# Performance work log

Hardware: AMD Instinct MI355X
Metric: run time of the kernel (lower is better)

The kernel has to match this reference:

```python
import jax, jax.numpy as jnp
import numpy as np

OUT, L, LPS, K = 256, 24, 6, 3          # classes, layers, layers_per_stack, kernel
RC, GC, SC, FC = 64, 128, 64, 80        # residual, gate, skip, feature channels
SCALES = (4, 4, 4, 4)                   # upsample scales, prod = 256 (hop size)
AUX = 2                                 # aux_context_window
B, T = 2, 16384
TF = T // int(np.prod(SCALES)) + 2 * AUX  # 68 mel frames fed in


def _conv1d(x, w, b=None, dilation=1, pad=(0, 0)):
    # x: (B,C,T), w: (O,C,K)
    y = jax.lax.conv_general_dilated(x, w, (1,), [pad], rhs_dilation=(dilation,),
                                     dimension_numbers=('NCH', 'OIH', 'NCH'))
    return y if b is None else y + b[None, :, None]


def _smooth(x, k):
    # depthwise-in-time smoothing: Conv2d(1,1,(1,Kk)) applied to (B,1,C,T)
    Bb, C, Tt = x.shape
    Kk = k.shape[0]
    y = jax.lax.conv_general_dilated(x.reshape(Bb * C, 1, Tt), k.reshape(1, 1, Kk),
                                     (1,), [(Kk // 2, Kk // 2)],
                                     dimension_numbers=('NCH', 'OIH', 'NCH'))
    return y.reshape(Bb, C, Tt)


def _wavenet(x, feature, first_W, first_b, conv_W, conv_b, cond_W,
             skip_W, skip_b, res_W, res_b, last1_W, last1_b, last2_W, last2_b,
             convin_W, up_K):
    # shift right by one (teacher forcing) then one-hot -> (B, OUT, T)
    xs = jnp.pad(x, ((0, 0), (1, 0)))[:, :-1]
    xoh = jax.nn.one_hot(xs, OUT, dtype=jnp.float32).transpose(0, 2, 1)

    # ConvInUpsampleNetwork: valid conv over aux context, then nearest-up + smooth
    f = _conv1d(feature, convin_W)  # (B, FC, TF - 2*AUX)
    for i, s in enumerate(SCALES):
        f = jnp.repeat(f, s, axis=-1)
        f = _smooth(f, up_K[i])
    # f: (B, FC, T)

    out = jnp.einsum('oc,bct->bot', first_W, xoh) + first_b[None, :, None]
    skips = jnp.zeros((x.shape[0], SC, x.shape[1]), jnp.float32)
    for l in range(L):
        d = 2 ** (l % LPS)
        pad = (K - 1) * d  # causal: left-pad only (== torch pad both + trim right)
        h = _conv1d(out, conv_W[l], conv_b[l], dilation=d, pad=(pad, 0))
        h = h + jnp.einsum('oc,bct->bot', cond_W[l], f)
        a, g = jnp.split(h, 2, axis=1)
        z = jnp.tanh(a) * jax.nn.sigmoid(g)  # (B, GC//2, T)
        skips = skips + jnp.einsum('oc,bct->bot', skip_W[l], z) + skip_b[l][None, :, None]
        out = jnp.einsum('oc,bct->bot', res_W[l], z) + res_b[l][None, :, None] + out
    h = jax.nn.relu(skips)
    h = jax.nn.relu(jnp.einsum('oc,bct->bot', last1_W, h) + last1_b[None, :, None])
    h = jnp.einsum('oc,bct->bot', last2_W, h) + last2_b[None, :, None]
    return h  # (B, OUT, T)


def setup_inputs() -> dict:
    key = jax.random.key(0)
    ks = jax.random.split(key, 12)
    s = 0.05
    return {
        'x': jax.random.randint(ks[0], (B, T), 0, OUT),
        'feature': jax.random.normal(ks[1], (B, FC, TF), jnp.float32),
        'first_W': jax.random.normal(ks[2], (RC, OUT), jnp.float32) * s,
        'first_b': jnp.zeros((RC,), jnp.float32),
        'conv_W': jax.random.normal(ks[3], (L, GC, RC, K), jnp.float32) * s,
        'conv_b': jnp.zeros((L, GC), jnp.float32),
        'cond_W': jax.random.normal(ks[4], (L, GC, FC), jnp.float32) * s,
        'skip_W': jax.random.normal(ks[5], (L, SC, GC // 2), jnp.float32) * s,
        'skip_b': jnp.zeros((L, SC), jnp.float32),
        'res_W': jax.random.normal(ks[6], (L, RC, GC // 2), jnp.float32) * s,
        'res_b': jnp.zeros((L, RC), jnp.float32),
        'last1_W': jax.random.normal(ks[7], (SC, SC), jnp.float32) * s,
        'last1_b': jnp.zeros((SC,), jnp.float32),
        'last2_W': jax.random.normal(ks[8], (OUT, SC), jnp.float32) * s,
        'last2_b': jnp.zeros((OUT,), jnp.float32),
        'convin_W': jax.random.normal(ks[9], (FC, FC, 2 * AUX + 1), jnp.float32) * s,
        'up_K': jnp.full((len(SCALES), 9), 1.0 / 9.0, jnp.float32),
    }


def reference(x, feature, first_W, first_b, conv_W, conv_b, cond_W,
              skip_W, skip_b, res_W, res_b, last1_W, last1_b, last2_W, last2_b,
              convin_W, up_K):
    return _wavenet(x, feature, first_W, first_b, conv_W, conv_b, cond_W,
                    skip_W, skip_b, res_W, res_b, last1_W, last1_b,
                    last2_W, last2_b, convin_W, up_K)
```

## Files before the change

### kernel.cpp

```cpp
#include <hip/hip_runtime.h>
#include <math.h>

#define T_LEN   16384
#define NB      2
#define FCH     80
#define NLAYERS 24
#define TFRAMES 68

typedef __attribute__((ext_vector_type(8))) short bf16x8;
typedef __attribute__((ext_vector_type(4))) float f32x4;

static __device__ inline unsigned short f2bf(float f) {
    unsigned int u = __float_as_uint(f);
    unsigned int r = (u + 0x7FFFu + ((u >> 16) & 1u)) >> 16;
    return (unsigned short)r;
}

__global__ void k_pack(const float* __restrict__ convW, const float* __restrict__ condW,
                       const float* __restrict__ skipW, const float* __restrict__ resW,
                       const float* __restrict__ last1W, const float* __restrict__ last2W,
                       const float* __restrict__ firstW, const float* __restrict__ firstb,
                       unsigned short* __restrict__ ATb, unsigned short* __restrict__ SRTb,
                       unsigned short* __restrict__ W1b, unsigned short* __restrict__ W2b,
                       float* __restrict__ firstWT) {
    int idx = blockIdx.x * 256 + threadIdx.x;
    const int nAT = NLAYERS * 128 * 288;
    const int nSR = NLAYERS * 128 * 64;
    const int e0 = nAT, e1 = e0 + nSR, e2 = e1 + 4096, e3 = e2 + 16384, e4 = e3 + 16384;
    if (idx < e0) {
        int k = idx % 288;
        int o = (idx / 288) & 127;
        int l = idx / (288 * 128);
        float v = 0.f;
        if (k < 192) v = convW[(((l * 128 + o) * 64) + (k & 63)) * 3 + (k >> 6)];
        else if (k - 192 < 80) v = condW[(l * 128 + o) * 80 + (k - 192)];
        ATb[idx] = f2bf(v);
    } else if (idx < e1) {
        int j = idx - e0;
        int k = j & 63;
        int o2 = (j >> 6) & 127;
        int l = j / (64 * 128);
        float v = (o2 < 64) ? skipW[(l * 64 + o2) * 64 + k]
                            : resW[(l * 64 + (o2 - 64)) * 64 + k];
        SRTb[j] = f2bf(v);
    } else if (idx < e2) {
        W1b[idx - e1] = f2bf(last1W[idx - e1]);
    } else if (idx < e3) {
        W2b[idx - e2] = f2bf(last2W[idx - e2]);
    } else if (idx < e4) {
        int j = idx - e3;
        int xs = j >> 6, c = j & 63;
        firstWT[j] = firstW[c * 256 + xs] + firstb[c];
    }
}

__global__ void k_convin(const float* __restrict__ feat, const float* __restrict__ W,
                         float* __restrict__ f0) {
    int idx = blockIdx.x * 256 + threadIdx.x;
    if (idx >= NB * FCH * 64) return;
    int t = idx & 63;
    int o = (idx >> 6) % FCH;
    int b = idx / (64 * FCH);
    const float* fb = feat + b * FCH * TFRAMES;
    const float* wo = W + o * FCH * 5;
    float acc = 0.f;
    for (int i = 0; i < FCH; ++i) {
        const float* fi = fb + i * TFRAMES + t;
        const float* wi = wo + i * 5;
#pragma unroll
        for (int k = 0; k < 5; ++k) acc += fi[k] * wi[k];
    }
    f0[idx] = acc;
}

__global__ void k_up(const float* __restrict__ in, float* __restrict__ out,
                     const float* __restrict__ kern, int Tin) {
    int Tout = Tin * 4;
    int idx = blockIdx.x * 256 + threadIdx.x;
    if (idx >= NB * FCH * Tout) return;
    int t = idx % Tout;
    int bc = idx / Tout;
    const float* ib = in + bc * Tin;
    float acc = 0.f;
#pragma unroll
    for (int k = 0; k < 9; ++k) {
        int u = t + k - 4;
        if (u >= 0 && u < Tout) acc += kern[k] * ib[u >> 2];
    }
    out[idx] = acc;
}

__global__ __launch_bounds__(256)
void k_up_last(const float* __restrict__ in, unsigned short* __restrict__ outH,
               const float* __restrict__ kern) {
    __shared__ float sF[18 * 80];
    const int tid = threadIdx.x;
    const int b  = blockIdx.x >> 8;
    const int t0 = (blockIdx.x & 255) * 64;
    const int fr0 = (t0 >> 2) - 1;

    for (int idx = tid; idx < 18 * 80; idx += 256) {
        int c = idx / 18, fr = idx - c * 18;
        int gfr = fr0 + fr;
        float v = 0.f;
        if (gfr >= 0 && gfr < 4096) v = in[((size_t)b * 80 + c) * 4096 + gfr];
        sF[fr * 80 + c] = v;
    }
    float kr[9];
#pragma unroll
    for (int k = 0; k < 9; ++k) kr[k] = kern[k];
    __syncthreads();

    for (int idx = tid; idx < 64 * 96; idx += 256) {
        int c = idx % 96;
        int t = idx / 96;
        float acc = 0.f;
        if (c < 80) {
            int ubase = t0 + t - 4;
#pragma unroll
            for (int k = 0; k < 9; ++k) {
                int fr = ((ubase + k) >> 2) - fr0;
                acc += kr[k] * sF[fr * 80 + c];
            }
        }
        outH[((size_t)b * T_LEN + t0 + t) * 96 + c] = f2bf(acc);
    }
}

__global__ __launch_bounds__(512, 1)
void k_stack(const int* __restrict__ x, const float* __restrict__ firstWT,
             const float* __restrict__ prevF, const unsigned short* __restrict__ prevH,
             float* __restrict__ nextF, unsigned short* __restrict__ nextH,
             float* __restrict__ skipF, const unsigned short* __restrict__ ffb,
             const unsigned short* __restrict__ ATb, const unsigned short* __restrict__ SRTb,
             const float* __restrict__ convB, const float* __restrict__ skipB,
             const float* __restrict__ resB,
             const unsigned short* __restrict__ W1b, const float* __restrict__ b1,
             const unsigned short* __restrict__ W2b, const float* __restrict__ b2,
             float* __restrict__ outp, int flags)
{
    __shared__ __align__(16) unsigned short s_A[264 * 72];
    __shared__ __align__(16) unsigned short s_B[264 * 72];
    __shared__ __align__(16) unsigned short s_Z[256 * 72];

    const int tid  = threadIdx.x;
    const int b    = blockIdx.x >> 7;
    const int t0   = (blockIdx.x & 127) * 128;
    const int lane = tid & 63;
    const int wv   = tid >> 6;
    const int col  = lane & 15;
    const int quad = lane >> 4;
    const int pair = wv & 3;
    const int par  = wv >> 2;
    const int chA  = 16 * pair + 4 * quad;
    const int srm  = (wv < 4) ? wv : (wv - 4);
    const int chS  = 16 * srm + 4 * quad;
    const bool firstStack = (flags & 1) != 0;
    const bool lastStack  = (flags & 2) != 0;

    const int ts_out[7] = {0, 0, 1, 2, 4, 8, 8};

    for (int i = tid; i < 144; i += 512) {
        int bufsel = (i >= 72);
        int j = i - bufsel * 72;
        int r = j / 9, seg = j - r * 9;
        bf16x8 zz = {0, 0, 0, 0, 0, 0, 0, 0};
        *(bf16x8*)((bufsel ? s_B : s_A) + r * 72 + seg * 8) = zz;
    }
    if (firstStack) {
        for (int i = tid; i < 256 * 8; i += 512) {
            int r = i >> 3, seg = i & 7;
            int g = t0 - 128 + r;
            bf16x8 v = {0, 0, 0, 0, 0, 0, 0, 0};
            if (g >= 0) {
                int xs = (g == 0) ? 0 : x[b * T_LEN + g - 1];
                const float* p = firstWT + xs * 64 + seg * 8;
                f32x4 a0 = *(const f32x4*)p;
                f32x4 a1 = *(const f32x4*)(p + 4);
                v[0] = (short)f2bf(a0[0]); v[1] = (short)f2bf(a0[1]);
                v[2] = (short)f2bf(a0[2]); v[3] = (short)f2bf(a0[3]);
                v[4] = (short)f2bf(a1[0]); v[5] = (short)f2bf(a1[1]);
                v[6] = (short)f2bf(a1[2]); v[7] = (short)f2bf(a1[3]);
            }
            *(bf16x8*)(s_A + (8 + r) * 72 + seg * 8) = v;
        }
    } else {
        const unsigned short* hb = prevH + (size_t)b * T_LEN * 64;
        for (int i = tid; i < 256 * 8; i += 512) {
            int r = i >> 3, seg = i & 7;
            int g = t0 - 128 + r;
            bf16x8 v = {0, 0, 0, 0, 0, 0, 0, 0};
            if (g >= 0) v = *(const bf16x8*)(hb + (size_t)g * 64 + seg * 8);
            *(bf16x8*)(s_A + (8 + r) * 72 + seg * 8) = v;
        }
    }

    f32x4 resReg[8];
    f32x4 skipAcc[8];
#pragma unroll
    for (int i = 0; i < 8; ++i) skipAcc[i] = (f32x4){0.f, 0.f, 0.f, 0.f};
    if (wv >= 4) {
        if (firstStack) {
#pragma unroll
            for (int i = 0; i < 8; ++i) {
                int t = t0 + i * 16 + col;
                int xs = (t == 0) ? 0 : x[b * T_LEN + t - 1];
                resReg[i] = *(const f32x4*)(firstWT + xs * 64 + chS);
            }
        } else {
#pragma unroll
            for (int i = 0; i < 8; ++i)
                resReg[i] = *(const f32x4*)(prevF +
                              ((size_t)b * T_LEN + t0 + i * 16 + col) * 64 + chS);
        }
    }
    __syncthreads();

    unsigned short* P = s_A;
    unsigned short* Q = s_B;

#pragma unroll 1
    for (int l = 0; l < 6; ++l) {
        const int d  = 1 << l;
        const int ts = ts_out[l];

        const unsigned short* AL = ATb + (size_t)l * 128 * 288;
        bf16x8 frA0[9], frA1[9];
#pragma unroll
        for (int ks = 0; ks < 9; ++ks) {
            frA0[ks] = *(const bf16x8*)(AL + (size_t)(16 * pair + col) * 288 + ks * 32 + quad * 8);
            frA1[ks] = *(const bf16x8*)(AL + (size_t)(64 + 16 * pair + col) * 288 + ks * 32 + quad * 8);
        }
        f32x4 cbA = *(const f32x4*)(convB + l * 128 + chA);
        f32x4 cbG = *(const f32x4*)(convB + l * 128 + 64 + chA);

#pragma unroll 1
        for (int tl = ts; tl < 16; ++tl) {
            if ((tl & 1) != par) continue;
            const int r_base = 8 + tl * 16 + col;
            int g = t0 - 128 + tl * 16 + col;
            int gcl = g < 0 ? 0 : g;
            const unsigned short* fc = ffb + ((size_t)b * T_LEN + gcl) * 96 + quad * 8;
            bf16x8 f6 = *(const bf16x8*)(fc);
            bf16x8 f7 = *(const bf16x8*)(fc + 32);
            bf16x8 f8 = *(const bf16x8*)(fc + 64);
            f32x4 a0 = (f32x4){0.f, 0.f, 0.f, 0.f};
            f32x4 a1 = (f32x4){0.f, 0.f, 0.f, 0.f};
#pragma unroll
            for (int ks = 0; ks < 6; ++ks) {
                int r_in = r_base - 2 * d + (ks >> 1) * d;
                bf16x8 fB = *(const bf16x8*)(P + r_in * 72 + (ks & 1) * 32 + quad * 8);
                a0 = __builtin_amdgcn_mfma_f32_16x16x32_bf16(frA0[ks], fB, a0, 0, 0, 0);
                a1 = __builtin_amdgcn_mfma_f32_16x16x32_bf16(frA1[ks], fB, a1, 0, 0, 0);
            }
            a0 = __builtin_amdgcn_mfma_f32_16x16x32_bf16(frA0[6], f6, a0, 0, 0, 0);
            a1 = __builtin_amdgcn_mfma_f32_16x16x32_bf16(frA1[6], f6, a1, 0, 0, 0);
            a0 = __builtin_amdgcn_mfma_f32_16x16x32_bf16(frA0[7], f7, a0, 0, 0, 0);
            a1 = __builtin_amdgcn_mfma_f32_16x16x32_bf16(frA1[7], f7, a1, 0, 0, 0);
            a0 = __builtin_amdgcn_mfma_f32_16x16x32_bf16(frA0[8], f8, a0, 0, 0, 0);
            a1 = __builtin_amdgcn_mfma_f32_16x16x32_bf16(frA1[8], f8, a1, 0, 0, 0);

            unsigned int pk[2];
#pragma unroll
            for (int r2 = 0; r2 < 2; ++r2) {
                float zz[2];
#pragma unroll
                for (int e = 0; e < 2; ++e) {
                    float av = a0[2 * r2 + e] + cbA[2 * r2 + e];
                    float gv = a1[2 * r2 + e] + cbG[2 * r2 + e];
                    float th = 1.f - 2.f * __builtin_amdgcn_rcpf(__expf(2.f * av) + 1.f);
                    float sg = __builtin_amdgcn_rcpf(1.f + __expf(-gv));
                    zz[e] = th * sg;
                }
                pk[r2] = (unsigned int)f2bf(zz[0]) | ((unsigned int)f2bf(zz[1]) << 16);
            }
            unsigned int* zp = (unsigned int*)(s_Z + (tl * 16 + col) * 72 + chA);
            zp[0] = pk[0];
            zp[1] = pk[1];
        }
        __syncthreads();

        const unsigned short* SL = SRTb + (size_t)l * 128 * 64;
        if (wv < 4) {
            bf16x8 wk0 = *(const bf16x8*)(SL + (size_t)(16 * srm + col) * 64 + quad * 8);
            bf16x8 wk1 = *(const bf16x8*)(SL + (size_t)(16 * srm + col) * 64 + 32 + quad * 8);
            f32x4 sb4 = *(const f32x4*)(skipB + l * 64 + chS);
#pragma unroll
            for (int i = 0; i < 8; ++i) {
                const int zr = ((8 + i) * 16 + col) * 72;
                bf16x8 fz0 = *(const bf16x8*)(s_Z + zr + quad * 8);
                bf16x8 fz1 = *(const bf16x8*)(s_Z + zr + 32 + quad * 8);
                f32x4 s = (f32x4){0.f, 0.f, 0.f, 0.f};
                s = __builtin_amdgcn_mfma_f32_16x16x32_bf16(wk0, fz0, s, 0, 0, 0);
                s = __builtin_amdgcn_mfma_f32_16x16x32_bf16(wk1, fz1, s, 0, 0, 0);
#pragma unroll
                for (int e = 0; e < 4; ++e) skipAcc[i][e] += s[e] + sb4[e];
            }
        } else {
            bf16x8 wr0 = *(const bf16x8*)(SL + (size_t)(64 + 16 * srm + col) * 64 + quad * 8);
            bf16x8 wr1 = *(const bf16x8*)(SL + (size_t)(64 + 16 * srm + col) * 64 + 32 + quad * 8);
            f32x4 rb4 = *(const f32x4*)(resB + l * 64 + chS);
#pragma unroll 1
            for (int tl = ts; tl < 8; ++tl) {
                const int zr = (tl * 16 + col) * 72;
                bf16x8 fz0 = *(const bf16x8*)(s_Z + zr + quad * 8);
                bf16x8 fz1 = *(const bf16x8*)(s_Z + zr + 32 + quad * 8);
                const int row = 8 + tl * 16 + col;
                const unsigned int* pv = (const unsigned int*)(P + row * 72 + chS);
                unsigned int w0 = pv[0], w1 = pv[1];
                f32x4 acc;
                acc[0] = __uint_as_float(w0 << 16);
                acc[1] = __uint_as_float(w0 & 0xFFFF0000u);
                acc[2] = __uint_as_float(w1 << 16);
                acc[3] = __uint_as_float(w1 & 0xFFFF0000u);
                acc = __builtin_amdgcn_mfma_f32_16x16x32_bf16(wr0, fz0, acc, 0, 0, 0);
                acc = __builtin_amdgcn_mfma_f32_16x16x32_bf16(wr1, fz1, acc, 0, 0, 0);
#pragma unroll
                for (int e = 0; e < 4; ++e) acc[e] += rb4[e];
                int g = t0 - 128 + tl * 16 + col;
                if (g < 0) acc = (f32x4){0.f, 0.f, 0.f, 0.f};
                unsigned int p01 = (unsigned int)f2bf(acc[0]) | ((unsigned int)f2bf(acc[1]) << 16);
                unsigned int p23 = (unsigned int)f2bf(acc[2]) | ((unsigned int)f2bf(acc[3]) << 16);
                unsigned int* qp = (unsigned int*)(Q + row * 72 + chS);
                qp[0] = p01;
                qp[1] = p23;
            }
            if (!(lastStack && l == 5)) {
#pragma unroll
                for (int i = 0; i < 8; ++i) {
                    const int zr = ((8 + i) * 16 + col) * 72;
                    bf16x8 fz0 = *(const bf16x8*)(s_Z + zr + quad * 8);
                    bf16x8 fz1 = *(const bf16x8*)(s_Z + zr + 32 + quad * 8);
                    f32x4 acc = resReg[i];
                    acc = __builtin_amdgcn_mfma_f32_16x16x32_bf16(wr0, fz0, acc, 0, 0, 0);
                    acc = __builtin_amdgcn_mfma_f32_16x16x32_bf16(wr1, fz1, acc, 0, 0, 0);
#pragma unroll
                    for (int e = 0; e < 4; ++e) acc[e] += rb4[e];
                    resReg[i] = acc;
                    if (l < 5) {
                        const int row = 8 + (8 + i) * 16 + col;
                        unsigned int p01 = (unsigned int)f2bf(acc[0]) | ((unsigned int)f2bf(acc[1]) << 16);
                        unsigned int p23 = (unsigned int)f2bf(acc[2]) | ((unsigned int)f2bf(acc[3]) << 16);
                        unsigned int* qp = (unsigned int*)(Q + row * 72 + chS);
                        qp[0] = p01;
                        qp[1] = p23;
                    }
                }
            }
        }
        __syncthreads();
        unsigned short* tmp = P; P = Q; Q = tmp;
    }

    if (!lastStack) {
        if (wv >= 4) {
#pragma unroll
            for (int i = 0; i < 8; ++i) {
                size_t base = ((size_t)b * T_LEN + t0 + i * 16 + col) * 64 + chS;
                *(f32x4*)(nextF + base) = resReg[i];
                unsigned int p01 = (unsigned int)f2bf(resReg[i][0]) | ((unsigned int)f2bf(resReg[i][1]) << 16);
                unsigned int p23 = (unsigned int)f2bf(resReg[i][2]) | ((unsigned int)f2bf(resReg[i][3]) << 16);
                unsigned int* hp = (unsigned int*)(nextH + base);
                hp[0] = p01;
                hp[1] = p23;
            }
        } else {
#pragma unroll
            for (int i = 0; i < 8; ++i) {
                size_t base = ((size_t)b * T_LEN + t0 + i * 16 + col) * 64 + chS;
                if (firstStack) {
                    *(f32x4*)(skipF + base) = skipAcc[i];
                } else {
                    f32x4 s = *(const f32x4*)(skipF + base);
#pragma unroll
                    for (int e = 0; e < 4; ++e) s[e] += skipAcc[i][e];
                    *(f32x4*)(skipF + base) = s;
                }
            }
        }
        return;
    }

    unsigned short* s_S = s_Z;
    unsigned short* s_H = s_Z + 128 * 72;
    if (wv < 4) {
#pragma unroll
        for (int i = 0; i < 8; ++i) {
            size_t base = ((size_t)b * T_LEN + t0 + i * 16 + col) * 64 + chS;
            f32x4 s = *(const f32x4*)(skipF + base);
            float v0 = fmaxf(s[0] + skipAcc[i][0], 0.f);
            float v1 = fmaxf(s[1] + skipAcc[i][1], 0.f);
            float v2 = fmaxf(s[2] + skipAcc[i][2], 0.f);
            float v3 = fmaxf(s[3] + skipAcc[i][3], 0.f);
            unsigned int* sp = (unsigned int*)(s_S + (i * 16 + col) * 72 + chS);
            sp[0] = (unsigned int)f2bf(v0) | ((unsigned int)f2bf(v1) << 16);
            sp[1] = (unsigned int)f2bf(v2) | ((unsigned int)f2bf(v3) << 16);
        }
    }
    __syncthreads();

    {
        const int m1 = wv & 3;
        const int q1 = wv >> 2;
        bf16x8 fw0 = *(const bf16x8*)(W1b + (size_t)(16 * m1 + col) * 64 + quad * 8);
        bf16x8 fw1 = *(const bf16x8*)(W1b + (size_t)(16 * m1 + col) * 64 + 32 + quad * 8);
        f32x4 bb1 = *(const f32x4*)(b1 + 16 * m1 + 4 * quad);
#pragma unroll
        for (int i = 0; i < 8; ++i) {
            if ((i & 1) != q1) continue;
            const int zr = (i * 16 + col) * 72;
            bf16x8 fz0 = *(const bf16x8*)(s_S + zr + quad * 8);
            bf16x8 fz1 = *(const bf16x8*)(s_S + zr + 32 + quad * 8);
            f32x4 a = (f32x4){0.f, 0.f, 0.f, 0.f};
            a = __builtin_amdgcn_mfma_f32_16x16x32_bf16(fw0, fz0, a, 0, 0, 0);
            a = __builtin_amdgcn_mfma_f32_16x16x32_bf16(fw1, fz1, a, 0, 0, 0);
            float h0 = fmaxf(a[0] + bb1[0], 0.f), h1 = fmaxf(a[1] + bb1[1], 0.f);
            float h2 = fmaxf(a[2] + bb1[2], 0.f), h3 = fmaxf(a[3] + bb1[3], 0.f);
            unsigned int* hp = (unsigned int*)(s_H + (i * 16 + col) * 72 + 16 * m1 + 4 * quad);
            hp[0] = (unsigned int)f2bf(h0) | ((unsigned int)f2bf(h1) << 16);
            hp[1] = (unsigned int)f2bf(h2) | ((unsigned int)f2bf(h3) << 16);
        }
    }
    __syncthreads();

#pragma unroll
    for (int p2 = 0; p2 < 2; ++p2) {
        const int m2 = wv + 8 * p2;
        bf16x8 fw0 = *(const bf16x8*)(W2b + (size_t)(16 * m2 + col) * 64 + quad * 8);
        bf16x8 fw1 = *(const bf16x8*)(W2b + (size_t)(16 * m2 + col) * 64 + 32 + quad * 8);
        f32x4 bb2 = *(const f32x4*)(b2 + 16 * m2 + 4 * quad);
#pragma unroll
        for (int i = 0; i < 8; ++i) {
            const int zr = (i * 16 + col) * 72;
            bf16x8 fz0 = *(const bf16x8*)(s_H + zr + quad * 8);
            bf16x8 fz1 = *(const bf16x8*)(s_H + zr + 32 + quad * 8);
            f32x4 a = (f32x4){0.f, 0.f, 0.f, 0.f};
            a = __builtin_amdgcn_mfma_f32_16x16x32_bf16(fw0, fz0, a, 0, 0, 0);
            a = __builtin_amdgcn_mfma_f32_16x16x32_bf16(fw1, fz1, a, 0, 0, 0);
            int t = t0 + i * 16 + col;
            int o0 = 16 * m2 + 4 * quad;
#pragma unroll
            for (int e = 0; e < 4; ++e)
                outp[((size_t)b * 256 + o0 + e) * T_LEN + t] = a[e] + bb2[e];
        }
    }
}

extern "C" void kernel_launch(void* const* d_in, const int* in_sizes, int n_in,
                              void* d_out, int out_size, void* d_ws, size_t ws_size,
                              hipStream_t stream) {
    const int*   x       = (const int*)  d_in[0];
    const float* feature = (const float*)d_in[1];
    const float* firstW  = (const float*)d_in[2];
    const float* firstb  = (const float*)d_in[3];
    const float* convW   = (const float*)d_in[4];
    const float* convB   = (const float*)d_in[5];
    const float* condW   = (const float*)d_in[6];
    const float* skipW   = (const float*)d_in[7];
    const float* skipB   = (const float*)d_in[8];
    const float* resW    = (const float*)d_in[9];
    const float* resB    = (const float*)d_in[10];
    const float* last1W  = (const float*)d_in[11];
    const float* last1b  = (const float*)d_in[12];
    const float* last2W  = (const float*)d_in[13];
    const float* last2b  = (const float*)d_in[14];
    const float* convinW = (const float*)d_in[15];
    const float* upK     = (const float*)d_in[16];

    float* ws = (float*)d_ws;
    float* f0      = ws;
    float* f1      = f0 + 10240;
    float* f2      = f1 + 40960;
    float* f3      = f2 + 163840;
    float* firstWT = f3 + 655360;
    float* resA    = firstWT + 16384;
    float* resB_   = resA + 2097152;
    float* skipF   = resB_ + 2097152;
    unsigned short* mirA = (unsigned short*)(skipF + 2097152);
    unsigned short* mirB = mirA + 2097152;
    unsigned short* ffb  = mirB + 2097152;
    unsigned short* ATb  = ffb + 3145728;
    unsigned short* SRTb = ATb + 884736;
    unsigned short* W1b  = SRTb + 196608;
    unsigned short* W2b  = W1b + 4096;

    int n;
    n = NLAYERS * 128 * 288 + NLAYERS * 128 * 64 + 4096 + 16384 + 16384;
    k_pack<<<(n + 255) / 256, 256, 0, stream>>>(convW, condW, skipW, resW, last1W, last2W,
                                                firstW, firstb, ATb, SRTb, W1b, W2b, firstWT);
    n = NB * FCH * 64;
    k_convin<<<(n + 255) / 256, 256, 0, stream>>>(feature, convinW, f0);
    k_up<<<(NB * FCH * 256 + 255) / 256, 256, 0, stream>>>(f0, f1, upK + 0, 64);
    k_up<<<(NB * FCH * 1024 + 255) / 256, 256, 0, stream>>>(f1, f2, upK + 9, 256);
    k_up<<<(NB * FCH * 4096 + 255) / 256, 256, 0, stream>>>(f2, f3, upK + 18, 1024);
    k_up_last<<<NB * 256, 256, 0, stream>>>(f3, ffb, upK + 27);

    float* poF = resA;          float* pnF = resB_;
    unsigned short* poH = mirA; unsigned short* pnH = mirB;
    for (int s = 0; s < 4; ++s) {
        int flags = (s == 0 ? 1 : 0) | (s == 3 ? 2 : 0);
        k_stack<<<NB * 128, 512, 0, stream>>>(
            x, firstWT, poF, poH, pnF, pnH, skipF, ffb,
            ATb + (size_t)s * 6 * 128 * 288, SRTb + (size_t)s * 6 * 128 * 64,
            convB + s * 6 * 128, skipB + s * 6 * 64, resB + s * 6 * 64,
            W1b, last1b, W2b, last2b, (float*)d_out, flags);
        float* tf = poF; poF = pnF; pnF = tf;
        unsigned short* th = poH; poH = pnH; pnH = th;
    }
}
```

Before: 393.2 us.

## Update residual buffer in place and rebalance skip/residual work across waves

Measured after the change: 791.0 us. +101.1%, slower.

```diff
diff --git a/kernel.cpp b/kernel.cpp
--- a/kernel.cpp
+++ b/kernel.cpp
@@ -6,6 +6,7 @@
 #define FCH     80
 #define NLAYERS 24
 #define TFRAMES 68
+#define PAD     76
 
 typedef __attribute__((ext_vector_type(8))) short bf16x8;
 typedef __attribute__((ext_vector_type(4))) float f32x4;
@@ -127,7 +128,7 @@
     }
 }
 
-__global__ __launch_bounds__(512, 1)
+__global__ __launch_bounds__(512, 4)
 void k_stack(const int* __restrict__ x, const float* __restrict__ firstWT,
              const float* __restrict__ prevF, const unsigned short* __restrict__ prevH,
              float* __restrict__ nextF, unsigned short* __restrict__ nextH,
@@ -139,9 +140,8 @@
              const unsigned short* __restrict__ W2b, const float* __restrict__ b2,
              float* __restrict__ outp, int flags)
 {
-    __shared__ __align__(16) unsigned short s_A[264 * 72];
-    __shared__ __align__(16) unsigned short s_B[264 * 72];
-    __shared__ __align__(16) unsigned short s_Z[256 * 72];
+    __shared__ __align__(16) unsigned short s_P[264 * PAD];
+    __shared__ __align__(16) unsigned short s_Z[256 * PAD];
 
     const int tid  = threadIdx.x;
     const int b    = blockIdx.x >> 7;
@@ -158,14 +158,11 @@
     const bool firstStack = (flags & 1) != 0;
     const bool lastStack  = (flags & 2) != 0;
 
-    const int ts_out[7] = {0, 0, 1, 2, 4, 8, 8};
-
-    for (int i = tid; i < 144; i += 512) {
-        int bufsel = (i >= 72);
-        int j = i - bufsel * 72;
-        int r = j / 9, seg = j - r * 9;
-        bf16x8 zz = {0, 0, 0, 0, 0, 0, 0, 0};
-        *(bf16x8*)((bufsel ? s_B : s_A) + r * 72 + seg * 8) = zz;
+    const int ts_out[6] = {0, 0, 1, 2, 4, 8};
+
+    for (int i = tid; i < 8 * (PAD / 2); i += 512) {
+        int r = i / (PAD / 2), dw = i - r * (PAD / 2);
+        ((unsigned int*)(s_P + r * PAD))[dw] = 0u;
     }
     if (firstStack) {
         for (int i = tid; i < 256 * 8; i += 512) {
@@ -182,7 +179,7 @@
                 v[4] = (short)f2bf(a1[0]); v[5] = (short)f2bf(a1[1]);
                 v[6] = (short)f2bf(a1[2]); v[7] = (short)f2bf(a1[3]);
             }
-            *(bf16x8*)(s_A + (8 + r) * 72 + seg * 8) = v;
+            *(bf16x8*)(s_P + (8 + r) * PAD + seg * 8) = v;
         }
     } else {
         const unsigned short* hb = prevH + (size_t)b * T_LEN * 64;
@@ -191,7 +188,7 @@
             int g = t0 - 128 + r;
             bf16x8 v = {0, 0, 0, 0, 0, 0, 0, 0};
             if (g >= 0) v = *(const bf16x8*)(hb + (size_t)g * 64 + seg * 8);
-            *(bf16x8*)(s_A + (8 + r) * 72 + seg * 8) = v;
+            *(bf16x8*)(s_P + (8 + r) * PAD + seg * 8) = v;
         }
     }
 
@@ -216,9 +213,6 @@
     }
     __syncthreads();
 
-    unsigned short* P = s_A;
-    unsigned short* Q = s_B;
-
 #pragma unroll 1
     for (int l = 0; l < 6; ++l) {
         const int d  = 1 << l;
@@ -234,9 +228,10 @@
         f32x4 cbA = *(const f32x4*)(convB + l * 128 + chA);
         f32x4 cbG = *(const f32x4*)(convB + l * 128 + 64 + chA);
 
-#pragma unroll 1
-        for (int tl = ts; tl < 16; ++tl) {
-            if ((tl & 1) != par) continue;
+#pragma unroll
+        for (int i8 = 0; i8 < 8; ++i8) {
+            const int tl = 2 * i8 + par;
+            if (tl < ts) continue;
             const int r_base = 8 + tl * 16 + col;
             int g = t0 - 128 + tl * 16 + col;
             int gcl = g < 0 ? 0 : g;
@@ -249,7 +244,7 @@
 #pragma unroll
             for (int ks = 0; ks < 6; ++ks) {
                 int r_in = r_base - 2 * d + (ks >> 1) * d;
-                bf16x8 fB = *(const bf16x8*)(P + r_in * 72 + (ks & 1) * 32 + quad * 8);
+                bf16x8 fB = *(const bf16x8*)(s_P + r_in * PAD + (ks & 1) * 32 + quad * 8);
                 a0 = __builtin_amdgcn_mfma_f32_16x16x32_bf16(frA0[ks], fB, a0, 0, 0, 0);
                 a1 = __builtin_amdgcn_mfma_f32_16x16x32_bf16(frA1[ks], fB, a1, 0, 0, 0);
             }
@@ -274,7 +269,7 @@
                 }
                 pk[r2] = (unsigned int)f2bf(zz[0]) | ((unsigned int)f2bf(zz[1]) << 16);
             }
-            unsigned int* zp = (unsigned int*)(s_Z + (tl * 16 + col) * 72 + chA);
+            unsigned int* zp = (unsigned int*)(s_Z + (tl * 16 + col) * PAD + chA);
             zp[0] = pk[0];
             zp[1] = pk[1];
         }
@@ -284,10 +279,13 @@
         if (wv < 4) {
             bf16x8 wk0 = *(const bf16x8*)(SL + (size_t)(16 * srm + col) * 64 + quad * 8);
             bf16x8 wk1 = *(const bf16x8*)(SL + (size_t)(16 * srm + col) * 64 + 32 + quad * 8);
+            bf16x8 wr0 = *(const bf16x8*)(SL + (size_t)(64 + 16 * srm + col) * 64 + quad * 8);
+            bf16x8 wr1 = *(const bf16x8*)(SL + (size_t)(64 + 16 * srm + col) * 64 + 32 + quad * 8);
             f32x4 sb4 = *(const f32x4*)(skipB + l * 64 + chS);
+            f32x4 rb4 = *(const f32x4*)(resB + l * 64 + chS);
 #pragma unroll
             for (int i = 0; i < 8; ++i) {
-                const int zr = ((8 + i) * 16 + col) * 72;
+                const int zr = ((8 + i) * 16 + col) * PAD;
                 bf16x8 fz0 = *(const bf16x8*)(s_Z + zr + quad * 8);
                 bf16x8 fz1 = *(const bf16x8*)(s_Z + zr + 32 + quad * 8);
                 f32x4 s = (f32x4){0.f, 0.f, 0.f, 0.f};
@@ -296,17 +294,14 @@
 #pragma unroll
                 for (int e = 0; e < 4; ++e) skipAcc[i][e] += s[e] + sb4[e];
             }
-        } else {
-            bf16x8 wr0 = *(const bf16x8*)(SL + (size_t)(64 + 16 * srm + col) * 64 + quad * 8);
-            bf16x8 wr1 = *(const bf16x8*)(SL + (size_t)(64 + 16 * srm + col) * 64 + 32 + quad * 8);
-            f32x4 rb4 = *(const f32x4*)(resB + l * 64 + chS);
-#pragma unroll 1
-            for (int tl = ts; tl < 8; ++tl) {
-                const int zr = (tl * 16 + col) * 72;
+#pragma unroll
+            for (int tl = 0; tl < 8; ++tl) {
+                if (tl < ts) continue;
+                const int zr = (tl * 16 + col) * PAD;
                 bf16x8 fz0 = *(const bf16x8*)(s_Z + zr + quad * 8);
                 bf16x8 fz1 = *(const bf16x8*)(s_Z + zr + 32 + quad * 8);
                 const int row = 8 + tl * 16 + col;
-                const unsigned int* pv = (const unsigned int*)(P + row * 72 + chS);
+                unsigned int* pv = (unsigned int*)(s_P + row * PAD + chS);
                 unsigned int w0 = pv[0], w1 = pv[1];
                 f32x4 acc;
                 acc[0] = __uint_as_float(w0 << 16);
@@ -319,16 +314,17 @@
                 for (int e = 0; e < 4; ++e) acc[e] += rb4[e];
                 int g = t0 - 128 + tl * 16 + col;
                 if (g < 0) acc = (f32x4){0.f, 0.f, 0.f, 0.f};
-                unsigned int p01 = (unsigned int)f2bf(acc[0]) | ((unsigned int)f2bf(acc[1]) << 16);
-                unsigned int p23 = (unsigned int)f2bf(acc[2]) | ((unsigned int)f2bf(acc[3]) << 16);
-                unsigned int* qp = (unsigned int*)(Q + row * 72 + chS);
-                qp[0] = p01;
-                qp[1] = p23;
-            }
+                pv[0] = (unsigned int)f2bf(acc[0]) | ((unsigned int)f2bf(acc[1]) << 16);
+                pv[1] = (unsigned int)f2bf(acc[2]) | ((unsigned int)f2bf(acc[3]) << 16);
+            }
+        } else {
             if (!(lastStack && l == 5)) {
+                bf16x8 wr0 = *(const bf16x8*)(SL + (size_t)(64 + 16 * srm + col) * 64 + quad * 8);
+                bf16x8 wr1 = *(const bf16x8*)(SL + (size_t)(64 + 16 * srm + col) * 64 + 32 + quad * 8);
+                f32x4 rb4 = *(const f32x4*)(resB + l * 64 + chS);
 #pragma unroll
                 for (int i = 0; i < 8; ++i) {
-                    const int zr = ((8 + i) * 16 + col) * 72;
+                    const int zr = ((8 + i) * 16 + col) * PAD;
                     bf16x8 fz0 = *(const bf16x8*)(s_Z + zr + quad * 8);
                     bf16x8 fz1 = *(const bf16x8*)(s_Z + zr + 32 + quad * 8);
                     f32x4 acc = resReg[i];
@@ -339,17 +335,14 @@
                     resReg[i] = acc;
                     if (l < 5) {
                         const int row = 8 + (8 + i) * 16 + col;
-                        unsigned int p01 = (unsigned int)f2bf(acc[0]) | ((unsigned int)f2bf(acc[1]) << 16);
-                        unsigned int p23 = (unsigned int)f2bf(acc[2]) | ((unsigned int)f2bf(acc[3]) << 16);
-                        unsigned int* qp = (unsigned int*)(Q + row * 72 + chS);
-                        qp[0] = p01;
-                        qp[1] = p23;
+                        unsigned int* qp = (unsigned int*)(s_P + row * PAD + chS);
+                        qp[0] = (unsigned int)f2bf(acc[0]) | ((unsigned int)f2bf(acc[1]) << 16);
+                        qp[1] = (unsigned int)f2bf(acc[2]) | ((unsigned int)f2bf(acc[3]) << 16);
                     }
                 }
             }
         }
         __syncthreads();
-        unsigned short* tmp = P; P = Q; Q = tmp;
     }
 
     if (!lastStack) {
@@ -382,7 +375,7 @@
     }
 
     unsigned short* s_S = s_Z;
-    unsigned short* s_H = s_Z + 128 * 72;
+    unsigned short* s_H = s_Z + 128 * PAD;
     if (wv < 4) {
 #pragma unroll
         for (int i = 0; i < 8; ++i) {
@@ -392,7 +385,7 @@
             float v1 = fmaxf(s[1] + skipAcc[i][1], 0.f);
             float v2 = fmaxf(s[2] + skipAcc[i][2], 0.f);
             float v3 = fmaxf(s[3] + skipAcc[i][3], 0.f);
-            unsigned int* sp = (unsigned int*)(s_S + (i * 16 + col) * 72 + chS);
+            unsigned int* sp = (unsigned int*)(s_S + (i * 16 + col) * PAD + chS);
             sp[0] = (unsigned int)f2bf(v0) | ((unsigned int)f2bf(v1) << 16);
             sp[1] = (unsigned int)f2bf(v2) | ((unsigned int)f2bf(v3) << 16);
         }
@@ -408,7 +401,7 @@
 #pragma unroll
         for (int i = 0; i < 8; ++i) {
             if ((i & 1) != q1) continue;
-            const int zr = (i * 16 + col) * 72;
+            const int zr = (i * 16 + col) * PAD;
             bf16x8 fz0 = *(const bf16x8*)(s_S + zr + quad * 8);
             bf16x8 fz1 = *(const bf16x8*)(s_S + zr + 32 + quad * 8);
             f32x4 a = (f32x4){0.f, 0.f, 0.f, 0.f};
@@ -416,7 +409,7 @@
             a = __builtin_amdgcn_mfma_f32_16x16x32_bf16(fw1, fz1, a, 0, 0, 0);
             float h0 = fmaxf(a[0] + bb1[0], 0.f), h1 = fmaxf(a[1] + bb1[1], 0.f);
             float h2 = fmaxf(a[2] + bb1[2], 0.f), h3 = fmaxf(a[3] + bb1[3], 0.f);
-            unsigned int* hp = (unsigned int*)(s_H + (i * 16 + col) * 72 + 16 * m1 + 4 * quad);
+            unsigned int* hp = (unsigned int*)(s_H + (i * 16 + col) * PAD + 16 * m1 + 4 * quad);
             hp[0] = (unsigned int)f2bf(h0) | ((unsigned int)f2bf(h1) << 16);
             hp[1] = (unsigned int)f2bf(h2) | ((unsigned int)f2bf(h3) << 16);
         }
@@ -431,7 +424,7 @@
         f32x4 bb2 = *(const f32x4*)(b2 + 16 * m2 + 4 * quad);
 #pragma unroll
         for (int i = 0; i < 8; ++i) {
-            const int zr = (i * 16 + col) * 72;
+            const int zr = (i * 16 + col) * PAD;
             bf16x8 fz0 = *(const bf16x8*)(s_H + zr + quad * 8);
             bf16x8 fz1 = *(const bf16x8*)(s_H + zr + 32 + quad * 8);
             f32x4 a = (f32x4){0.f, 0.f, 0.f, 0.f};
```
